# Optimization experiments

Measured on AMD Instinct MI355X. Metric: run time of the kernel, lower is better.

The kernel has to match this reference:

```python
import jax, jax.numpy as jnp
import numpy as np

N = 50000
E = 800000
D_IN, D_HID, D_OUT = 128, 128, 64


def setup_inputs() -> dict:
    key = jax.random.key(0)
    ks = jax.random.split(key, 8)
    x = jax.random.normal(ks[0], (N, D_IN), dtype=jnp.float32)
    edge_index = jax.random.randint(ks[1], (2, E), 0, N, dtype=jnp.int64)
    # Glorot-ish init for GCNConv linear weights + zero bias (PyG default bias=True)
    def lin(k, din, dout):
        s = 1.0 / np.sqrt(din)
        return jax.random.uniform(k, (din, dout), jnp.float32, -s, s)
    return {
        "x": x,
        "edge_index": edge_index,
        "W1": lin(ks[2], D_IN, D_HID), "b1": jnp.zeros((D_HID,), jnp.float32),
        "W2": lin(ks[3], D_HID, D_HID), "b2": jnp.zeros((D_HID,), jnp.float32),
        "W3": lin(ks[4], D_HID, D_OUT), "b3": jnp.zeros((D_OUT,), jnp.float32),
    }


def _prep_edges(edge_index, n):
    # add self loops (PyG GCNConv default add_self_loops=True)
    loop = jnp.arange(n, dtype=edge_index.dtype)
    src = jnp.concatenate([edge_index[0], loop])
    dst = jnp.concatenate([edge_index[1], loop])
    deg = jax.ops.segment_sum(jnp.ones_like(dst, dtype=jnp.float32), dst, num_segments=n)
    dinv = jnp.where(deg > 0, jax.lax.rsqrt(deg), 0.0)
    norm = dinv[src] * dinv[dst]  # symmetric normalization per edge
    return src, dst, norm


def _gcn_conv(h, W, b, src, dst, norm, n):
    h = h @ W                                   # [N, dout]
    msg = h[src] * norm[:, None]                # [E+N, dout] gather
    out = jax.ops.segment_sum(msg, dst, num_segments=n)  # scatter-add
    return out + b


def reference(x, edge_index, W1, b1, W2, b2, W3, b3):
    src, dst, norm = _prep_edges(edge_index, N)
    h = jax.nn.relu(_gcn_conv(x, W1, b1, src, dst, norm, N))
    h = jax.nn.relu(_gcn_conv(h, W2, b2, src, dst, norm, N))
    return _gcn_conv(h, W3, b3, src, dst, norm, N)  # eval mode: dropout is identity
```

## Files before the change

kernel.cpp:

```cpp
#include <hip/hip_runtime.h>
#include <hip/hip_fp16.h>
#include <math.h>

#define NN 50000
#define NE 800000
#define RAWSTRIDE 96
#define NBUCK 196
#define NBBIN 196
#define BCAP 4608
#define ACH 4096
#define G1B 782

using bf8v = __attribute__((ext_vector_type(8))) short;
using f4v  = __attribute__((ext_vector_type(4))) float;

__device__ inline unsigned short f2bf(float f) {
    unsigned int u = __float_as_uint(f);
    u += 0x7FFFu + ((u >> 16) & 1u);
    return (unsigned short)(u >> 16);
}
__device__ inline float bflo(unsigned int d) { return __uint_as_float(d << 16); }
__device__ inline float bfhi(unsigned int d) { return __uint_as_float(d & 0xFFFF0000u); }


__device__ __forceinline__ void bin_body(const int* __restrict__ src,
                                         const int* __restrict__ dst,
                                         int* __restrict__ gcursor,
                                         unsigned int* __restrict__ bst,
                                         int bx, char* shc) {
    unsigned int* items = (unsigned int*)shc;
    int* cnt    = (int*)(shc + 16384);
    int* pref   = (int*)(shc + 17408);
    int* gstart = (int*)(shc + 18436);
    const int t = threadIdx.x;
    cnt[t] = 0;
    __syncthreads();
    const int base = bx * ACH;

    unsigned int my[16]; int myb[16], myr[16];
    #pragma unroll
    for (int i = 0; i < 16; ++i) {
        int e = base + i * 256 + t;
        my[i] = 0; myb[i] = -1; myr[i] = 0;
        if (e < NE) {
            int d = dst[e], s = src[e];
            my[i] = (unsigned int)s | ((unsigned int)d << 16);
            int b = d >> 8;
            myb[i] = b;
            myr[i] = atomicAdd(&cnt[b], 1);
        }
    }
    __syncthreads();
    if (t == 0) {
        int run = 0;
        for (int b = 0; b < 256; ++b) { pref[b] = run; run += cnt[b]; }
        pref[256] = run;
    }
    __syncthreads();
    if (cnt[t] > 0) gstart[t] = atomicAdd(&gcursor[t], cnt[t]);
    __syncthreads();
    #pragma unroll
    for (int i = 0; i < 16; ++i)
        if (myb[i] >= 0) items[pref[myb[i]] + myr[i]] = my[i];
    __syncthreads();
    const int total = pref[256];
    for (int i = t; i < total; i += 256) {
        int lo = 0, hi = 255;
        while (lo < hi) { int mid = (lo + hi + 1) >> 1; if (pref[mid] <= i) lo = mid; else hi = mid - 1; }
        int idx = gstart[lo] + (i - pref[lo]);
        if (idx < BCAP) bst[(size_t)lo * BCAP + idx] = items[i];
    }
}


__global__ __launch_bounds__(512) void sortb_kernel(const int* __restrict__ gcursor,
                                                    const unsigned int* __restrict__ bst,
                                                    int* __restrict__ cnt_g,
                                                    float* __restrict__ dinv,
                                                    unsigned short* __restrict__ raw) {
    __shared__ unsigned int items[BCAP];
    __shared__ int cnt[256], pref[257], cur[256];
    __shared__ unsigned short outl[BCAP];
    const int b = blockIdx.x;
    const int t = threadIdx.x;
    int n = gcursor[b];
    if (n > BCAP) n = BCAP;
    if (t < 256) { cnt[t] = 0; cur[t] = 0; }
    __syncthreads();
    for (int i = t; i < n; i += 512) {
        unsigned int u = bst[(size_t)b * BCAP + i];
        items[i] = u;
        atomicAdd(&cnt[(u >> 16) & 255], 1);
    }
    __syncthreads();
    if (t == 0) {
        int run = 0;
        for (int j = 0; j < 256; ++j) { pref[j] = run; run += cnt[j]; }
        pref[256] = run;
    }
    __syncthreads();
    for (int i = t; i < n; i += 512) {
        unsigned int u = items[i];
        int ln = (u >> 16) & 255;
        int r = atomicAdd(&cur[ln], 1);
        outl[pref[ln] + r] = (unsigned short)(u & 0xFFFFu);
    }
    __syncthreads();
    for (int i = t; i < n; i += 512) {
        int lo = 0, hi = 255;
        while (lo < hi) { int mid = (lo + hi + 1) >> 1; if (pref[mid] <= i) lo = mid; else hi = mid - 1; }
        int r = i - pref[lo];
        if (r < RAWSTRIDE) raw[(size_t)(b * 256 + lo) * RAWSTRIDE + r] = outl[i];
    }
    if (t < 256) {
        int node = b * 256 + t;
        if (node < NN) {
            int c = cnt[t];
            cnt_g[node] = c;
            dinv[node] = rsqrtf((float)(1 + c));
        }
    }
}


template <bool A_FP32>
__device__ __forceinline__ void gemm128_body(const void* __restrict__ Ain,
                                             const float* __restrict__ W,
                                             unsigned short* __restrict__ out,
                                             int bx, char* shc) {
    unsigned short* Wt = (unsigned short*)shc;
    unsigned short* Dt = (unsigned short*)(shc + 128 * 136 * 2);
    const int t = threadIdx.x;
    const int row0 = bx * 64;

    {
        int n = t & 127;
        int kbase = (t >> 7) * 4;
        for (int kk = kbase; kk < 128; kk += 8) {
            float w0 = W[(kk + 0) * 128 + n];
            float w1 = W[(kk + 1) * 128 + n];
            float w2 = W[(kk + 2) * 128 + n];
            float w3 = W[(kk + 3) * 128 + n];
            unsigned int p0 = (unsigned int)f2bf(w0) | ((unsigned int)f2bf(w1) << 16);
            unsigned int p1 = (unsigned int)f2bf(w2) | ((unsigned int)f2bf(w3) << 16);
            *(unsigned int*)&Wt[n * 136 + kk]     = p0;
            *(unsigned int*)&Wt[n * 136 + kk + 2] = p1;
        }
    }
    __syncthreads();

    const int wave = t >> 6;
    const int lane = t & 63;
    const int m16  = lane & 15;
    const int quad = lane >> 4;
    const int arow = row0 + wave * 16 + m16;
    const int arowc = (arow < NN) ? arow : 0;

    f4v acc[8];
    #pragma unroll
    for (int i = 0; i < 8; ++i) acc[i] = (f4v)(0.0f);

    #pragma unroll
    for (int k0 = 0; k0 < 128; k0 += 32) {
        bf8v afrag;
        if (A_FP32) {
            const float* A = (const float*)Ain;
            const float4* ap = (const float4*)(A + (size_t)arowc * 128 + k0 + quad * 8);
            float4 a0 = ap[0], a1 = ap[1];
            afrag[0] = (short)f2bf(a0.x); afrag[1] = (short)f2bf(a0.y);
            afrag[2] = (short)f2bf(a0.z); afrag[3] = (short)f2bf(a0.w);
            afrag[4] = (short)f2bf(a1.x); afrag[5] = (short)f2bf(a1.y);
            afrag[6] = (short)f2bf(a1.z); afrag[7] = (short)f2bf(a1.w);
        } else {
            const unsigned short* A = (const unsigned short*)Ain;
            afrag = *(const bf8v*)(A + (size_t)arowc * 128 + k0 + quad * 8);
        }
        #pragma unroll
        for (int nt = 0; nt < 8; ++nt) {
            bf8v bfrag = *(const bf8v*)&Wt[(nt * 16 + m16) * 136 + k0 + quad * 8];
            acc[nt] = __builtin_amdgcn_mfma_f32_16x16x32_bf16(afrag, bfrag, acc[nt], 0, 0, 0);
        }
    }

    #pragma unroll
    for (int nt = 0; nt < 8; ++nt) {
        #pragma unroll
        for (int r = 0; r < 4; ++r) {
            Dt[(wave * 16 + quad * 4 + r) * 136 + nt * 16 + m16] = f2bf(acc[nt][r]);
        }
    }
    __syncthreads();

    {
        int r = t >> 2;
        int c = t & 3;
        int gr = row0 + r;
        if (gr < NN) {
            const uint4* s = (const uint4*)&Dt[r * 136] + c * 4;
            uint4* d = (uint4*)(out + (size_t)gr * 128) + c * 4;
            d[0] = s[0]; d[1] = s[1]; d[2] = s[2]; d[3] = s[3];
        }
    }
}

__global__ __launch_bounds__(256) void bin_g1_kernel(const int* __restrict__ src,
                                                     const int* __restrict__ dst,
                                                     int* __restrict__ gcursor,
                                                     unsigned int* __restrict__ bst,
                                                     const float* __restrict__ x,
                                                     const float* __restrict__ W1,
                                                     unsigned short* __restrict__ hb) {
    __shared__ __align__(16) char sh[52224];
    if (blockIdx.x < NBBIN) {
        bin_body(src, dst, gcursor, bst, blockIdx.x, sh);
    } else {
        gemm128_body<true>(x, W1, hb, blockIdx.x - NBBIN, sh);
    }
}

__global__ __launch_bounds__(256) void mfma_gemm_kernel(const unsigned short* __restrict__ Ain,
                                                        const float* __restrict__ W,
                                                        unsigned short* __restrict__ out) {
    __shared__ __align__(16) char sh[52224];
    gemm128_body<false>(Ain, W, out, blockIdx.x, sh);
}


template <bool RELU>
__global__ __launch_bounds__(256) void agg_bf16_kernel(const unsigned short* __restrict__ hin,
                                                       const unsigned short* __restrict__ raw,
                                                       const int* __restrict__ cnt_g,
                                                       const float* __restrict__ dinv,
                                                       const float* __restrict__ bias,
                                                       unsigned short* __restrict__ outb) {
    const int t = threadIdx.x;
    const int group = t >> 4;
    const int lane  = t & 15;
    const int wid = blockIdx.x * 16 + group;
    if (wid >= NN) return;

    int c = cnt_g[wid];
    if (c > RAWSTRIDE) c = RAWSTRIDE;
    const float diw = dinv[wid];
    const unsigned short* rrow = raw + (size_t)wid * RAWSTRIDE;
    const uint4* hv = (const uint4*)hin;

    float acc[8];
    {
        uint4 g = hv[(size_t)wid * 16 + lane];
        float ws = diw * diw;
        acc[0] = ws * bflo(g.x); acc[1] = ws * bfhi(g.x);
        acc[2] = ws * bflo(g.y); acc[3] = ws * bfhi(g.y);
        acc[4] = ws * bflo(g.z); acc[5] = ws * bfhi(g.z);
        acc[6] = ws * bflo(g.w); acc[7] = ws * bfhi(g.w);
    }

    #define ACCUM(G, W_) \
        acc[0] += W_ * bflo(G.x); acc[1] += W_ * bfhi(G.x); \
        acc[2] += W_ * bflo(G.y); acc[3] += W_ * bfhi(G.y); \
        acc[4] += W_ * bflo(G.z); acc[5] += W_ * bfhi(G.z); \
        acc[6] += W_ * bflo(G.w); acc[7] += W_ * bfhi(G.w);

    const int cfull = c & ~7;
    uint4 q;
    if (cfull > 0) q = *(const uint4*)(rrow);
    for (int e = 0; e < cfull; e += 8) {
        uint4 qc = q;
        if (e + 8 < cfull) q = *(const uint4*)(rrow + e + 8);
        int c0 = qc.x & 0xFFFFu, c1 = qc.x >> 16;
        int c2 = qc.y & 0xFFFFu, c3 = qc.y >> 16;
        int c4 = qc.z & 0xFFFFu, c5 = qc.z >> 16;
        int c6 = qc.w & 0xFFFFu, c7 = qc.w >> 16;
        uint4 g0 = hv[(size_t)c0 * 16 + lane];
        uint4 g1 = hv[(size_t)c1 * 16 + lane];
        uint4 g2 = hv[(size_t)c2 * 16 + lane];
        uint4 g3 = hv[(size_t)c3 * 16 + lane];
        uint4 g4 = hv[(size_t)c4 * 16 + lane];
        uint4 g5 = hv[(size_t)c5 * 16 + lane];
        uint4 g6 = hv[(size_t)c6 * 16 + lane];
        uint4 g7 = hv[(size_t)c7 * 16 + lane];
        float w0 = diw * dinv[c0], w1 = diw * dinv[c1];
        float w2 = diw * dinv[c2], w3 = diw * dinv[c3];
        float w4 = diw * dinv[c4], w5 = diw * dinv[c5];
        float w6 = diw * dinv[c6], w7 = diw * dinv[c7];
        ACCUM(g0, w0) ACCUM(g1, w1) ACCUM(g2, w2) ACCUM(g3, w3)
        ACCUM(g4, w4) ACCUM(g5, w5) ACCUM(g6, w6) ACCUM(g7, w7)
    }
    if (c & 7) {
        int e = cfull, rem = c - e;
        uint4 qc = *(const uint4*)(rrow + e);
        int c0 = qc.x & 0xFFFFu, c1 = qc.x >> 16;
        int c2 = qc.y & 0xFFFFu, c3 = qc.y >> 16;
        int c4 = qc.z & 0xFFFFu, c5 = qc.z >> 16;
        int c6 = qc.w & 0xFFFFu, c7 = qc.w >> 16;
        if (rem <= 1) c1 = 0; if (rem <= 2) c2 = 0; if (rem <= 3) c3 = 0;
        if (rem <= 4) c4 = 0; if (rem <= 5) c5 = 0; if (rem <= 6) c6 = 0;
        c7 = 0;
        float w0 = diw * dinv[c0];
        float w1 = (rem > 1) ? diw * dinv[c1] : 0.f;
        float w2 = (rem > 2) ? diw * dinv[c2] : 0.f;
        float w3 = (rem > 3) ? diw * dinv[c3] : 0.f;
        float w4 = (rem > 4) ? diw * dinv[c4] : 0.f;
        float w5 = (rem > 5) ? diw * dinv[c5] : 0.f;
        float w6 = (rem > 6) ? diw * dinv[c6] : 0.f;
        float w7 = 0.f;
        uint4 g0 = hv[(size_t)c0 * 16 + lane];
        uint4 g1 = hv[(size_t)c1 * 16 + lane];
        uint4 g2 = hv[(size_t)c2 * 16 + lane];
        uint4 g3 = hv[(size_t)c3 * 16 + lane];
        uint4 g4 = hv[(size_t)c4 * 16 + lane];
        uint4 g5 = hv[(size_t)c5 * 16 + lane];
        uint4 g6 = hv[(size_t)c6 * 16 + lane];
        uint4 g7 = hv[(size_t)c7 * 16 + lane];
        ACCUM(g0, w0) ACCUM(g1, w1) ACCUM(g2, w2) ACCUM(g3, w3)
        ACCUM(g4, w4) ACCUM(g5, w5) ACCUM(g6, w6) ACCUM(g7, w7)
    }
    #undef ACCUM

    const float4* bp = (const float4*)bias;
    float4 b0 = bp[lane * 2], b1 = bp[lane * 2 + 1];
    acc[0] += b0.x; acc[1] += b0.y; acc[2] += b0.z; acc[3] += b0.w;
    acc[4] += b1.x; acc[5] += b1.y; acc[6] += b1.z; acc[7] += b1.w;
    if (RELU) {
        #pragma unroll
        for (int j = 0; j < 8; ++j) acc[j] = fmaxf(acc[j], 0.f);
    }
    uint4 o;
    o.x = (unsigned int)f2bf(acc[0]) | ((unsigned int)f2bf(acc[1]) << 16);
    o.y = (unsigned int)f2bf(acc[2]) | ((unsigned int)f2bf(acc[3]) << 16);
    o.z = (unsigned int)f2bf(acc[4]) | ((unsigned int)f2bf(acc[5]) << 16);
    o.w = (unsigned int)f2bf(acc[6]) | ((unsigned int)f2bf(acc[7]) << 16);
    ((uint4*)(outb + (size_t)wid * 128))[lane] = o;
}


__global__ __launch_bounds__(256) void gemm3_kernel(const unsigned short* __restrict__ Ab,
                                                    const float* __restrict__ W,
                                                    unsigned short* __restrict__ outh) {
    constexpr int CG = 16;
    constexpr int RPT = 4;
    constexpr int ROWS = 64;
    constexpr int LD = 132;
    __shared__ float lds[ROWS * LD];
    const int t = threadIdx.x;
    const int row0 = blockIdx.x * ROWS;

    #pragma unroll
    for (int j = 0; j < ROWS / 8; ++j) {
        int idx4 = j * 256 + t;
        int r = idx4 >> 5, c4 = idx4 & 31;
        int gr = row0 + r;
        uint2 u = make_uint2(0u, 0u);
        if (gr < NN) u = ((const uint2*)(Ab + (size_t)gr * 128))[c4];
        float4 v;
        v.x = bflo(u.x); v.y = bfhi(u.x); v.z = bflo(u.y); v.w = bfhi(u.y);
        ((float4*)(lds + r * LD))[c4] = v;
    }
    __syncthreads();

    const int cg = t % CG;
    const int rt = t / CG;
    const float4* Wv = (const float4*)W;
    float4 acc[RPT];
    #pragma unroll
    for (int i = 0; i < RPT; ++i) acc[i] = make_float4(0.f, 0.f, 0.f, 0.f);

    for (int k0 = 0; k0 < 128; k0 += 4) {
        float4 w0 = Wv[(k0 + 0) * CG + cg];
        float4 w1 = Wv[(k0 + 1) * CG + cg];
        float4 w2 = Wv[(k0 + 2) * CG + cg];
        float4 w3 = Wv[(k0 + 3) * CG + cg];
        #pragma unroll
        for (int i = 0; i < RPT; ++i) {
            const float* lr = lds + (rt * RPT + i) * LD;
            float4 a = ((const float4*)lr)[k0 >> 2];
            acc[i].x += a.x * w0.x + a.y * w1.x + a.z * w2.x + a.w * w3.x;
            acc[i].y += a.x * w0.y + a.y * w1.y + a.z * w2.y + a.w * w3.y;
            acc[i].z += a.x * w0.z + a.y * w1.z + a.z * w2.z + a.w * w3.z;
            acc[i].w += a.x * w0.w + a.y * w1.w + a.z * w2.w + a.w * w3.w;
        }
    }

    #pragma unroll
    for (int i = 0; i < RPT; ++i) {
        int gr = row0 + rt * RPT + i;
        if (gr < NN) {
            uint2 o;
            o.x = (unsigned int)f2bf(acc[i].x) | ((unsigned int)f2bf(acc[i].y) << 16);
            o.y = (unsigned int)f2bf(acc[i].z) | ((unsigned int)f2bf(acc[i].w) << 16);
            ((uint2*)(outh + (size_t)gr * 64))[cg] = o;
        }
    }
}


__global__ __launch_bounds__(256) void agg3_kernel(const unsigned short* __restrict__ hin,
                                                   const unsigned short* __restrict__ raw,
                                                   const int* __restrict__ cnt_g,
                                                   const float* __restrict__ dinv,
                                                   const float* __restrict__ bias,
                                                   float* __restrict__ out) {
    const int t = threadIdx.x;
    const int group = t >> 3;
    const int lane  = t & 7;
    const int wid = blockIdx.x * 32 + group;
    if (wid >= NN) return;

    int c = cnt_g[wid];
    if (c > RAWSTRIDE) c = RAWSTRIDE;
    const float diw = dinv[wid];
    const unsigned short* rrow = raw + (size_t)wid * RAWSTRIDE;
    const uint4* hv = (const uint4*)hin;

    float acc[8];
    {
        uint4 g = hv[(size_t)wid * 8 + lane];
        float ws = diw * diw;
        acc[0] = ws * bflo(g.x); acc[1] = ws * bfhi(g.x);
        acc[2] = ws * bflo(g.y); acc[3] = ws * bfhi(g.y);
        acc[4] = ws * bflo(g.z); acc[5] = ws * bfhi(g.z);
        acc[6] = ws * bflo(g.w); acc[7] = ws * bfhi(g.w);
    }

    #define ACCUM(G, W_) \
        acc[0] += W_ * bflo(G.x); acc[1] += W_ * bfhi(G.x); \
        acc[2] += W_ * bflo(G.y); acc[3] += W_ * bfhi(G.y); \
        acc[4] += W_ * bflo(G.z); acc[5] += W_ * bfhi(G.z); \
        acc[6] += W_ * bflo(G.w); acc[7] += W_ * bfhi(G.w);

    const int cfull = c & ~7;
    uint4 q;
    if (cfull > 0) q = *(const uint4*)(rrow);
    for (int e = 0; e < cfull; e += 8) {
        uint4 qc = q;
        if (e + 8 < cfull) q = *(const uint4*)(rrow + e + 8);
        int c0 = qc.x & 0xFFFFu, c1 = qc.x >> 16;
        int c2 = qc.y & 0xFFFFu, c3 = qc.y >> 16;
        int c4 = qc.z & 0xFFFFu, c5 = qc.z >> 16;
        int c6 = qc.w & 0xFFFFu, c7 = qc.w >> 16;
        uint4 g0 = hv[(size_t)c0 * 8 + lane];
        uint4 g1 = hv[(size_t)c1 * 8 + lane];
        uint4 g2 = hv[(size_t)c2 * 8 + lane];
        uint4 g3 = hv[(size_t)c3 * 8 + lane];
        uint4 g4 = hv[(size_t)c4 * 8 + lane];
        uint4 g5 = hv[(size_t)c5 * 8 + lane];
        uint4 g6 = hv[(size_t)c6 * 8 + lane];
        uint4 g7 = hv[(size_t)c7 * 8 + lane];
        float w0 = diw * dinv[c0], w1 = diw * dinv[c1];
        float w2 = diw * dinv[c2], w3 = diw * dinv[c3];
        float w4 = diw * dinv[c4], w5 = diw * dinv[c5];
        float w6 = diw * dinv[c6], w7 = diw * dinv[c7];
        ACCUM(g0, w0) ACCUM(g1, w1) ACCUM(g2, w2) ACCUM(g3, w3)
        ACCUM(g4, w4) ACCUM(g5, w5) ACCUM(g6, w6) ACCUM(g7, w7)
    }
    if (c & 7) {
        int e = cfull, rem = c - e;
        uint4 qc = *(const uint4*)(rrow + e);
        int c0 = qc.x & 0xFFFFu, c1 = qc.x >> 16;
        int c2 = qc.y & 0xFFFFu, c3 = qc.y >> 16;
        int c4 = qc.z & 0xFFFFu, c5 = qc.z >> 16;
        int c6 = qc.w & 0xFFFFu, c7 = qc.w >> 16;
        if (rem <= 1) c1 = 0; if (rem <= 2) c2 = 0; if (rem <= 3) c3 = 0;
        if (rem <= 4) c4 = 0; if (rem <= 5) c5 = 0; if (rem <= 6) c6 = 0;
        c7 = 0;
        float w0 = diw * dinv[c0];
        float w1 = (rem > 1) ? diw * dinv[c1] : 0.f;
        float w2 = (rem > 2) ? diw * dinv[c2] : 0.f;
        float w3 = (rem > 3) ? diw * dinv[c3] : 0.f;
        float w4 = (rem > 4) ? diw * dinv[c4] : 0.f;
        float w5 = (rem > 5) ? diw * dinv[c5] : 0.f;
        float w6 = (rem > 6) ? diw * dinv[c6] : 0.f;
        float w7 = 0.f;
        uint4 g0 = hv[(size_t)c0 * 8 + lane];
        uint4 g1 = hv[(size_t)c1 * 8 + lane];
        uint4 g2 = hv[(size_t)c2 * 8 + lane];
        uint4 g3 = hv[(size_t)c3 * 8 + lane];
        uint4 g4 = hv[(size_t)c4 * 8 + lane];
        uint4 g5 = hv[(size_t)c5 * 8 + lane];
        uint4 g6 = hv[(size_t)c6 * 8 + lane];
        uint4 g7 = hv[(size_t)c7 * 8 + lane];
        ACCUM(g0, w0) ACCUM(g1, w1) ACCUM(g2, w2) ACCUM(g3, w3)
        ACCUM(g4, w4) ACCUM(g5, w5) ACCUM(g6, w6) ACCUM(g7, w7)
    }
    #undef ACCUM

    const float4* bp = (const float4*)bias;
    float4 b0 = bp[lane * 2], b1 = bp[lane * 2 + 1];
    acc[0] += b0.x; acc[1] += b0.y; acc[2] += b0.z; acc[3] += b0.w;
    acc[4] += b1.x; acc[5] += b1.y; acc[6] += b1.z; acc[7] += b1.w;

    float4 o0 = make_float4(acc[0], acc[1], acc[2], acc[3]);
    float4 o1 = make_float4(acc[4], acc[5], acc[6], acc[7]);
    ((float4*)(out + (size_t)wid * 64))[lane * 2]     = o0;
    ((float4*)(out + (size_t)wid * 64))[lane * 2 + 1] = o1;
}


extern "C" void kernel_launch(void* const* d_in, const int* in_sizes, int n_in,
                              void* d_out, int out_size, void* d_ws, size_t ws_size,
                              hipStream_t stream) {
    const float* x  = (const float*)d_in[0];
    const int*   ei = (const int*)d_in[1];
    const float* W1 = (const float*)d_in[2];
    const float* b1 = (const float*)d_in[3];
    const float* W2 = (const float*)d_in[4];
    const float* b2 = (const float*)d_in[5];
    const float* W3 = (const float*)d_in[6];
    const float* b3 = (const float*)d_in[7];
    float* out = (float*)d_out;

    char* w = (char*)d_ws;
    int*   cnt_g   = (int*)  (w + 0x0000000);
    int*   gcursor = (int*)  (w + 0x0040000);
    float* dinv    = (float*)(w + 0x0048000);
    unsigned int*   bst = (unsigned int*)  (w + 0x0080000);
    unsigned short* raw = (unsigned short*)(w + 0x0400000);
    unsigned short* hb  = (unsigned short*)(w + 0x0E00000);
    unsigned short* zb  = (unsigned short*)(w + 0x1B00000);
    unsigned short* h3b = (unsigned short*)(w + 0x2800000);

    const int* src = ei;
    const int* dst = ei + NE;

    hipMemsetAsync(gcursor, 0, NBUCK * sizeof(int), stream);
    bin_g1_kernel<<<NBBIN + G1B, 256, 0, stream>>>(src, dst, gcursor, bst, x, W1, hb);
    sortb_kernel<<<NBUCK, 512, 0, stream>>>(gcursor, bst, cnt_g, dinv, raw);
    agg_bf16_kernel<true><<<(NN + 15) / 16, 256, 0, stream>>>(hb, raw, cnt_g, dinv, b1, zb);
    mfma_gemm_kernel<<<G1B, 256, 0, stream>>>(zb, W2, hb);
    agg_bf16_kernel<true><<<(NN + 15) / 16, 256, 0, stream>>>(hb, raw, cnt_g, dinv, b2, zb);
    gemm3_kernel<<<G1B, 256, 0, stream>>>(zb, W3, h3b);
    agg3_kernel<<<(NN + 31) / 32, 256, 0, stream>>>(h3b, raw, cnt_g, dinv, b3, out);
}
```

Baseline: 246.7 us.

## Fuse aggregation with following GEMM in layers one and two

Layer-1 aggregation (with bias and ReLU) is merged with the W2 MFMA GEMM into one kernel, and layer-2 aggregation is merged with the W3 GEMM. Aggregated rows now stay in LDS instead of being written to global memory and read back, which also removes two kernel launches. In exchange, each block handles 64 rows serially in four passes of 16, so there are fewer blocks to hide gather latency, the W tile is rebuilt per block, and LDS use per block goes up.

```diff
diff --git a/kernel.cpp b/kernel.cpp
--- a/kernel.cpp
+++ b/kernel.cpp
@@ -123,11 +123,10 @@
 }
 
 
-template <bool A_FP32>
-__device__ __forceinline__ void gemm128_body(const void* __restrict__ Ain,
-                                             const float* __restrict__ W,
-                                             unsigned short* __restrict__ out,
-                                             int bx, char* shc) {
+__device__ __forceinline__ void gemm128_body_f32(const float* __restrict__ A,
+                                                 const float* __restrict__ W,
+                                                 unsigned short* __restrict__ out,
+                                                 int bx, char* shc) {
     unsigned short* Wt = (unsigned short*)shc;
     unsigned short* Dt = (unsigned short*)(shc + 128 * 136 * 2);
     const int t = threadIdx.x;
@@ -163,18 +162,12 @@
     #pragma unroll
     for (int k0 = 0; k0 < 128; k0 += 32) {
         bf8v afrag;
-        if (A_FP32) {
-            const float* A = (const float*)Ain;
-            const float4* ap = (const float4*)(A + (size_t)arowc * 128 + k0 + quad * 8);
-            float4 a0 = ap[0], a1 = ap[1];
-            afrag[0] = (short)f2bf(a0.x); afrag[1] = (short)f2bf(a0.y);
-            afrag[2] = (short)f2bf(a0.z); afrag[3] = (short)f2bf(a0.w);
-            afrag[4] = (short)f2bf(a1.x); afrag[5] = (short)f2bf(a1.y);
-            afrag[6] = (short)f2bf(a1.z); afrag[7] = (short)f2bf(a1.w);
-        } else {
-            const unsigned short* A = (const unsigned short*)Ain;
-            afrag = *(const bf8v*)(A + (size_t)arowc * 128 + k0 + quad * 8);
-        }
+        const float4* ap = (const float4*)(A + (size_t)arowc * 128 + k0 + quad * 8);
+        float4 a0 = ap[0], a1 = ap[1];
+        afrag[0] = (short)f2bf(a0.x); afrag[1] = (short)f2bf(a0.y);
+        afrag[2] = (short)f2bf(a0.z); afrag[3] = (short)f2bf(a0.w);
+        afrag[4] = (short)f2bf(a1.x); afrag[5] = (short)f2bf(a1.y);
+        afrag[6] = (short)f2bf(a1.z); afrag[7] = (short)f2bf(a1.w);
         #pragma unroll
         for (int nt = 0; nt < 8; ++nt) {
             bf8v bfrag = *(const bf8v*)&Wt[(nt * 16 + m16) * 136 + k0 + quad * 8];
@@ -214,150 +207,220 @@
     if (blockIdx.x < NBBIN) {
         bin_body(src, dst, gcursor, bst, blockIdx.x, sh);
     } else {
-        gemm128_body<true>(x, W1, hb, blockIdx.x - NBBIN, sh);
-    }
-}
-
-__global__ __launch_bounds__(256) void mfma_gemm_kernel(const unsigned short* __restrict__ Ain,
-                                                        const float* __restrict__ W,
-                                                        unsigned short* __restrict__ out) {
-    __shared__ __align__(16) char sh[52224];
-    gemm128_body<false>(Ain, W, out, blockIdx.x, sh);
-}
-
-
-template <bool RELU>
-__global__ __launch_bounds__(256) void agg_bf16_kernel(const unsigned short* __restrict__ hin,
-                                                       const unsigned short* __restrict__ raw,
-                                                       const int* __restrict__ cnt_g,
-                                                       const float* __restrict__ dinv,
-                                                       const float* __restrict__ bias,
-                                                       unsigned short* __restrict__ outb) {
+        gemm128_body_f32(x, W1, hb, blockIdx.x - NBBIN, sh);
+    }
+}
+
+
+#define AGG128_BODY(HV, RROW, C, DIW, LANE, ACCV)                                   \
+    {                                                                               \
+        uint4 g = HV[(size_t)wid * 16 + (LANE)];                                    \
+        float ws = (DIW) * (DIW);                                                   \
+        ACCV[0] = ws * bflo(g.x); ACCV[1] = ws * bfhi(g.x);                         \
+        ACCV[2] = ws * bflo(g.y); ACCV[3] = ws * bfhi(g.y);                         \
+        ACCV[4] = ws * bflo(g.z); ACCV[5] = ws * bfhi(g.z);                         \
+        ACCV[6] = ws * bflo(g.w); ACCV[7] = ws * bfhi(g.w);                         \
+    }                                                                               \
+    const int cfull = (C) & ~7;                                                     \
+    uint4 q;                                                                        \
+    if (cfull > 0) q = *(const uint4*)(RROW);                                       \
+    for (int e = 0; e < cfull; e += 8) {                                            \
+        uint4 qc = q;                                                               \
+        if (e + 8 < cfull) q = *(const uint4*)((RROW) + e + 8);                     \
+        int c0 = qc.x & 0xFFFFu, c1 = qc.x >> 16;                                   \
+        int c2 = qc.y & 0xFFFFu, c3 = qc.y >> 16;                                   \
+        int c4 = qc.z & 0xFFFFu, c5 = qc.z >> 16;                                   \
+        int c6 = qc.w & 0xFFFFu, c7 = qc.w >> 16;                                   \
+        uint4 g0 = HV[(size_t)c0 * 16 + (LANE)];                                    \
+        uint4 g1 = HV[(size_t)c1 * 16 + (LANE)];                                    \
+        uint4 g2 = HV[(size_t)c2 * 16 + (LANE)];                                    \
+        uint4 g3 = HV[(size_t)c3 * 16 + (LANE)];                                    \
+        uint4 g4 = HV[(size_t)c4 * 16 + (LANE)];                                    \
+        uint4 g5 = HV[(size_t)c5 * 16 + (LANE)];                                    \
+        uint4 g6 = HV[(size_t)c6 * 16 + (LANE)];                                    \
+        uint4 g7 = HV[(size_t)c7 * 16 + (LANE)];                                    \
+        float w0 = (DIW) * dinv[c0], w1 = (DIW) * dinv[c1];                         \
+        float w2 = (DIW) * dinv[c2], w3 = (DIW) * dinv[c3];                         \
+        float w4 = (DIW) * dinv[c4], w5 = (DIW) * dinv[c5];                         \
+        float w6 = (DIW) * dinv[c6], w7 = (DIW) * dinv[c7];                         \
+        ACC8(g0, w0) ACC8(g1, w1) ACC8(g2, w2) ACC8(g3, w3)                         \
+        ACC8(g4, w4) ACC8(g5, w5) ACC8(g6, w6) ACC8(g7, w7)                         \
+    }                                                                               \
+    if ((C) & 7) {                                                                  \
+        int e = cfull, rem = (C) - e;                                               \
+        uint4 qc = *(const uint4*)((RROW) + e);                                     \
+        int c0 = qc.x & 0xFFFFu, c1 = qc.x >> 16;                                   \
+        int c2 = qc.y & 0xFFFFu, c3 = qc.y >> 16;                                   \
+        int c4 = qc.z & 0xFFFFu, c5 = qc.z >> 16;                                   \
+        int c6 = qc.w & 0xFFFFu, c7 = qc.w >> 16;                                   \
+        if (rem <= 1) c1 = 0; if (rem <= 2) c2 = 0; if (rem <= 3) c3 = 0;           \
+        if (rem <= 4) c4 = 0; if (rem <= 5) c5 = 0; if (rem <= 6) c6 = 0;           \
+        c7 = 0;                                                                     \
+        float w0 = (DIW) * dinv[c0];                                                \
+        float w1 = (rem > 1) ? (DIW) * dinv[c1] : 0.f;                              \
+        float w2 = (rem > 2) ? (DIW) * dinv[c2] : 0.f;                              \
+        float w3 = (rem > 3) ? (DIW) * dinv[c3] : 0.f;                              \
+        float w4 = (rem > 4) ? (DIW) * dinv[c4] : 0.f;                              \
+        float w5 = (rem > 5) ? (DIW) * dinv[c5] : 0.f;                              \
+        float w6 = (rem > 6) ? (DIW) * dinv[c6] : 0.f;                              \
+        float w7 = 0.f;                                                             \
+        uint4 g0 = HV[(size_t)c0 * 16 + (LANE)];                                    \
+        uint4 g1 = HV[(size_t)c1 * 16 + (LANE)];                                    \
+        uint4 g2 = HV[(size_t)c2 * 16 + (LANE)];                                    \
+        uint4 g3 = HV[(size_t)c3 * 16 + (LANE)];                                    \
+        uint4 g4 = HV[(size_t)c4 * 16 + (LANE)];                                    \
+        uint4 g5 = HV[(size_t)c5 * 16 + (LANE)];                                    \
+        uint4 g6 = HV[(size_t)c6 * 16 + (LANE)];                                    \
+        uint4 g7 = HV[(size_t)c7 * 16 + (LANE)];                                    \
+        ACC8(g0, w0) ACC8(g1, w1) ACC8(g2, w2) ACC8(g3, w3)                         \
+        ACC8(g4, w4) ACC8(g5, w5) ACC8(g6, w6) ACC8(g7, w7)                         \
+    }
+
+#define ACC8(G, W_) \
+    acc[0] += W_ * bflo(G.x); acc[1] += W_ * bfhi(G.x); \
+    acc[2] += W_ * bflo(G.y); acc[3] += W_ * bfhi(G.y); \
+    acc[4] += W_ * bflo(G.z); acc[5] += W_ * bfhi(G.z); \
+    acc[6] += W_ * bflo(G.w); acc[7] += W_ * bfhi(G.w);
+
+
+__global__ __launch_bounds__(256) void aggW2_kernel(const unsigned short* __restrict__ hin,
+                                                    const unsigned short* __restrict__ raw,
+                                                    const int* __restrict__ cnt_g,
+                                                    const float* __restrict__ dinv,
+                                                    const float* __restrict__ bias,
+                                                    const float* __restrict__ W,
+                                                    unsigned short* __restrict__ out) {
+    __shared__ unsigned short Wt[128 * 136];
+    __shared__ unsigned short Zt[64 * 136];
     const int t = threadIdx.x;
+    const int row0 = blockIdx.x * 64;
+
+    {
+        int n = t & 127;
+        int kbase = (t >> 7) * 4;
+        for (int kk = kbase; kk < 128; kk += 8) {
+            float w0 = W[(kk + 0) * 128 + n];
+            float w1 = W[(kk + 1) * 128 + n];
+            float w2 = W[(kk + 2) * 128 + n];
+            float w3 = W[(kk + 3) * 128 + n];
+            unsigned int p0 = (unsigned int)f2bf(w0) | ((unsigned int)f2bf(w1) << 16);
+            unsigned int p1 = (unsigned int)f2bf(w2) | ((unsigned int)f2bf(w3) << 16);
+            *(unsigned int*)&Wt[n * 136 + kk]     = p0;
+            *(unsigned int*)&Wt[n * 136 + kk + 2] = p1;
+        }
+    }
+
     const int group = t >> 4;
     const int lane  = t & 15;
-    const int wid = blockIdx.x * 16 + group;
-    if (wid >= NN) return;
-
-    int c = cnt_g[wid];
-    if (c > RAWSTRIDE) c = RAWSTRIDE;
-    const float diw = dinv[wid];
-    const unsigned short* rrow = raw + (size_t)wid * RAWSTRIDE;
     const uint4* hv = (const uint4*)hin;
-
-    float acc[8];
-    {
-        uint4 g = hv[(size_t)wid * 16 + lane];
-        float ws = diw * diw;
-        acc[0] = ws * bflo(g.x); acc[1] = ws * bfhi(g.x);
-        acc[2] = ws * bflo(g.y); acc[3] = ws * bfhi(g.y);
-        acc[4] = ws * bflo(g.z); acc[5] = ws * bfhi(g.z);
-        acc[6] = ws * bflo(g.w); acc[7] = ws * bfhi(g.w);
-    }
-
-    #define ACCUM(G, W_) \
-        acc[0] += W_ * bflo(G.x); acc[1] += W_ * bfhi(G.x); \
-        acc[2] += W_ * bflo(G.y); acc[3] += W_ * bfhi(G.y); \
-        acc[4] += W_ * bflo(G.z); acc[5] += W_ * bfhi(G.z); \
-        acc[6] += W_ * bflo(G.w); acc[7] += W_ * bfhi(G.w);
-
-    const int cfull = c & ~7;
-    uint4 q;
-    if (cfull > 0) q = *(const uint4*)(rrow);
-    for (int e = 0; e < cfull; e += 8) {
-        uint4 qc = q;
-        if (e + 8 < cfull) q = *(const uint4*)(rrow + e + 8);
-        int c0 = qc.x & 0xFFFFu, c1 = qc.x >> 16;
-        int c2 = qc.y & 0xFFFFu, c3 = qc.y >> 16;
-        int c4 = qc.z & 0xFFFFu, c5 = qc.z >> 16;
-        int c6 = qc.w & 0xFFFFu, c7 = qc.w >> 16;
-        uint4 g0 = hv[(size_t)c0 * 16 + lane];
-        uint4 g1 = hv[(size_t)c1 * 16 + lane];
-        uint4 g2 = hv[(size_t)c2 * 16 + lane];
-        uint4 g3 = hv[(size_t)c3 * 16 + lane];
-        uint4 g4 = hv[(size_t)c4 * 16 + lane];
-        uint4 g5 = hv[(size_t)c5 * 16 + lane];
-        uint4 g6 = hv[(size_t)c6 * 16 + lane];
-        uint4 g7 = hv[(size_t)c7 * 16 + lane];
-        float w0 = diw * dinv[c0], w1 = diw * dinv[c1];
-        float w2 = diw * dinv[c2], w3 = diw * dinv[c3];
-        float w4 = diw * dinv[c4], w5 = diw * dinv[c5];
-        float w6 = diw * dinv[c6], w7 = diw * dinv[c7];
-        ACCUM(g0, w0) ACCUM(g1, w1) ACCUM(g2, w2) ACCUM(g3, w3)
-        ACCUM(g4, w4) ACCUM(g5, w5) ACCUM(g6, w6) ACCUM(g7, w7)
-    }
-    if (c & 7) {
-        int e = cfull, rem = c - e;
-        uint4 qc = *(const uint4*)(rrow + e);
-        int c0 = qc.x & 0xFFFFu, c1 = qc.x >> 16;
-        int c2 = qc.y & 0xFFFFu, c3 = qc.y >> 16;
-        int c4 = qc.z & 0xFFFFu, c5 = qc.z >> 16;
-        int c6 = qc.w & 0xFFFFu, c7 = qc.w >> 16;
-        if (rem <= 1) c1 = 0; if (rem <= 2) c2 = 0; if (rem <= 3) c3 = 0;
-        if (rem <= 4) c4 = 0; if (rem <= 5) c5 = 0; if (rem <= 6) c6 = 0;
-        c7 = 0;
-        float w0 = diw * dinv[c0];
-        float w1 = (rem > 1) ? diw * dinv[c1] : 0.f;
-        float w2 = (rem > 2) ? diw * dinv[c2] : 0.f;
-        float w3 = (rem > 3) ? diw * dinv[c3] : 0.f;
-        float w4 = (rem > 4) ? diw * dinv[c4] : 0.f;
-        float w5 = (rem > 5) ? diw * dinv[c5] : 0.f;
-        float w6 = (rem > 6) ? diw * dinv[c6] : 0.f;
-        float w7 = 0.f;
-        uint4 g0 = hv[(size_t)c0 * 16 + lane];
-        uint4 g1 = hv[(size_t)c1 * 16 + lane];
-        uint4 g2 = hv[(size_t)c2 * 16 + lane];
-        uint4 g3 = hv[(size_t)c3 * 16 + lane];
-        uint4 g4 = hv[(size_t)c4 * 16 + lane];
-        uint4 g5 = hv[(size_t)c5 * 16 + lane];
-        uint4 g6 = hv[(size_t)c6 * 16 + lane];
-        uint4 g7 = hv[(size_t)c7 * 16 + lane];
-        ACCUM(g0, w0) ACCUM(g1, w1) ACCUM(g2, w2) ACCUM(g3, w3)
-        ACCUM(g4, w4) ACCUM(g5, w5) ACCUM(g6, w6) ACCUM(g7, w7)
-    }
-    #undef ACCUM
-
     const float4* bp = (const float4*)bias;
     float4 b0 = bp[lane * 2], b1 = bp[lane * 2 + 1];
-    acc[0] += b0.x; acc[1] += b0.y; acc[2] += b0.z; acc[3] += b0.w;
-    acc[4] += b1.x; acc[5] += b1.y; acc[6] += b1.z; acc[7] += b1.w;
-    if (RELU) {
+
+    for (int r = 0; r < 4; ++r) {
+        const int wid = row0 + r * 16 + group;
+        uint4 o = make_uint4(0u, 0u, 0u, 0u);
+        if (wid < NN) {
+            int c = cnt_g[wid];
+            if (c > RAWSTRIDE) c = RAWSTRIDE;
+            const float diw = dinv[wid];
+            const unsigned short* rrow = raw + (size_t)wid * RAWSTRIDE;
+            float acc[8];
+            AGG128_BODY(hv, rrow, c, diw, lane, acc)
+            acc[0] += b0.x; acc[1] += b0.y; acc[2] += b0.z; acc[3] += b0.w;
+            acc[4] += b1.x; acc[5] += b1.y; acc[6] += b1.z; acc[7] += b1.w;
+            #pragma unroll
+            for (int j = 0; j < 8; ++j) acc[j] = fmaxf(acc[j], 0.f);
+            o.x = (unsigned int)f2bf(acc[0]) | ((unsigned int)f2bf(acc[1]) << 16);
+            o.y = (unsigned int)f2bf(acc[2]) | ((unsigned int)f2bf(acc[3]) << 16);
+            o.z = (unsigned int)f2bf(acc[4]) | ((unsigned int)f2bf(acc[5]) << 16);
+            o.w = (unsigned int)f2bf(acc[6]) | ((unsigned int)f2bf(acc[7]) << 16);
+        }
+        *(uint4*)&Zt[(r * 16 + group) * 136 + lane * 8] = o;
+    }
+    __syncthreads();
+
+    const int wave = t >> 6;
+    const int l64  = t & 63;
+    const int m16  = l64 & 15;
+    const int quad = l64 >> 4;
+
+    f4v acc[8];
+    #pragma unroll
+    for (int i = 0; i < 8; ++i) acc[i] = (f4v)(0.0f);
+
+    #pragma unroll
+    for (int k0 = 0; k0 < 128; k0 += 32) {
+        bf8v afrag = *(const bf8v*)&Zt[(wave * 16 + m16) * 136 + k0 + quad * 8];
         #pragma unroll
-        for (int j = 0; j < 8; ++j) acc[j] = fmaxf(acc[j], 0.f);
-    }
-    uint4 o;
-    o.x = (unsigned int)f2bf(acc[0]) | ((unsigned int)f2bf(acc[1]) << 16);
-    o.y = (unsigned int)f2bf(acc[2]) | ((unsigned int)f2bf(acc[3]) << 16);
-    o.z = (unsigned int)f2bf(acc[4]) | ((unsigned int)f2bf(acc[5]) << 16);
-    o.w = (unsigned int)f2bf(acc[6]) | ((unsigned int)f2bf(acc[7]) << 16);
-    ((uint4*)(outb + (size_t)wid * 128))[lane] = o;
-}
-
-
-__global__ __launch_bounds__(256) void gemm3_kernel(const unsigned short* __restrict__ Ab,
+        for (int nt = 0; nt < 8; ++nt) {
+            bf8v bfrag = *(const bf8v*)&Wt[(nt * 16 + m16) * 136 + k0 + quad * 8];
+            acc[nt] = __builtin_amdgcn_mfma_f32_16x16x32_bf16(afrag, bfrag, acc[nt], 0, 0, 0);
+        }
+    }
+    __syncthreads();
+
+    #pragma unroll
+    for (int nt = 0; nt < 8; ++nt) {
+        #pragma unroll
+        for (int r = 0; r < 4; ++r) {
+            Zt[(wave * 16 + quad * 4 + r) * 136 + nt * 16 + m16] = f2bf(acc[nt][r]);
+        }
+    }
+    __syncthreads();
+
+    {
+        int r = t >> 2;
+        int c = t & 3;
+        int gr = row0 + r;
+        if (gr < NN) {
+            const uint4* s = (const uint4*)&Zt[r * 136] + c * 4;
+            uint4* d = (uint4*)(out + (size_t)gr * 128) + c * 4;
+            d[0] = s[0]; d[1] = s[1]; d[2] = s[2]; d[3] = s[3];
+        }
+    }
+}
+
+
+__global__ __launch_bounds__(256) void aggG3_kernel(const unsigned short* __restrict__ hin,
+                                                    const unsigned short* __restrict__ raw,
+                                                    const int* __restrict__ cnt_g,
+                                                    const float* __restrict__ dinv,
+                                                    const float* __restrict__ bias,
                                                     const float* __restrict__ W,
                                                     unsigned short* __restrict__ outh) {
+    constexpr int LD = 132;
+    __shared__ float Zt[64 * LD];
+    const int t = threadIdx.x;
+    const int row0 = blockIdx.x * 64;
+
+    const int group = t >> 4;
+    const int lane  = t & 15;
+    const uint4* hv = (const uint4*)hin;
+    const float4* bp = (const float4*)bias;
+    float4 b0 = bp[lane * 2], b1 = bp[lane * 2 + 1];
+
+    for (int r = 0; r < 4; ++r) {
+        const int wid = row0 + r * 16 + group;
+        float acc[8] = {0.f, 0.f, 0.f, 0.f, 0.f, 0.f, 0.f, 0.f};
+        if (wid < NN) {
+            int c = cnt_g[wid];
+            if (c > RAWSTRIDE) c = RAWSTRIDE;
+            const float diw = dinv[wid];
+            const unsigned short* rrow = raw + (size_t)wid * RAWSTRIDE;
+            AGG128_BODY(hv, rrow, c, diw, lane, acc)
+            acc[0] += b0.x; acc[1] += b0.y; acc[2] += b0.z; acc[3] += b0.w;
+            acc[4] += b1.x; acc[5] += b1.y; acc[6] += b1.z; acc[7] += b1.w;
+            #pragma unroll
+            for (int j = 0; j < 8; ++j) acc[j] = fmaxf(acc[j], 0.f);
+        }
+        float4* zr = (float4*)&Zt[(r * 16 + group) * LD + lane * 8];
+        zr[0] = make_float4(acc[0], acc[1], acc[2], acc[3]);
+        zr[1] = make_float4(acc[4], acc[5], acc[6], acc[7]);
+    }
+    __syncthreads();
+
     constexpr int CG = 16;
     constexpr int RPT = 4;
-    constexpr int ROWS = 64;
-    constexpr int LD = 132;
-    __shared__ float lds[ROWS * LD];
-    const int t = threadIdx.x;
-    const int row0 = blockIdx.x * ROWS;
-
-    #pragma unroll
-    for (int j = 0; j < ROWS / 8; ++j) {
-        int idx4 = j * 256 + t;
-        int r = idx4 >> 5, c4 = idx4 & 31;
-        int gr = row0 + r;
-        uint2 u = make_uint2(0u, 0u);
-        if (gr < NN) u = ((const uint2*)(Ab + (size_t)gr * 128))[c4];
-        float4 v;
-        v.x = bflo(u.x); v.y = bfhi(u.x); v.z = bflo(u.y); v.w = bfhi(u.y);
-        ((float4*)(lds + r * LD))[c4] = v;
-    }
-    __syncthreads();
-
     const int cg = t % CG;
     const int rt = t / CG;
     const float4* Wv = (const float4*)W;
@@ -372,7 +435,7 @@
         float4 w3 = Wv[(k0 + 3) * CG + cg];
         #pragma unroll
         for (int i = 0; i < RPT; ++i) {
-            const float* lr = lds + (rt * RPT + i) * LD;
+            const float* lr = Zt + (rt * RPT + i) * LD;
             float4 a = ((const float4*)lr)[k0 >> 2];
             acc[i].x += a.x * w0.x + a.y * w1.x + a.z * w2.x + a.w * w3.x;
             acc[i].y += a.x * w0.y + a.y * w1.y + a.z * w2.y + a.w * w3.y;
@@ -421,12 +484,6 @@
         acc[4] = ws * bflo(g.z); acc[5] = ws * bfhi(g.z);
         acc[6] = ws * bflo(g.w); acc[7] = ws * bfhi(g.w);
     }
-
-    #define ACCUM(G, W_) \
-        acc[0] += W_ * bflo(G.x); acc[1] += W_ * bfhi(G.x); \
-        acc[2] += W_ * bflo(G.y); acc[3] += W_ * bfhi(G.y); \
-        acc[4] += W_ * bflo(G.z); acc[5] += W_ * bfhi(G.z); \
-        acc[6] += W_ * bflo(G.w); acc[7] += W_ * bfhi(G.w);
 
     const int cfull = c & ~7;
     uint4 q;
@@ -450,8 +507,8 @@
         float w2 = diw * dinv[c2], w3 = diw * dinv[c3];
         float w4 = diw * dinv[c4], w5 = diw * dinv[c5];
         float w6 = diw * dinv[c6], w7 = diw * dinv[c7];
-        ACCUM(g0, w0) ACCUM(g1, w1) ACCUM(g2, w2) ACCUM(g3, w3)
-        ACCUM(g4, w4) ACCUM(g5, w5) ACCUM(g6, w6) ACCUM(g7, w7)
+        ACC8(g0, w0) ACC8(g1, w1) ACC8(g2, w2) ACC8(g3, w3)
+        ACC8(g4, w4) ACC8(g5, w5) ACC8(g6, w6) ACC8(g7, w7)
     }
     if (c & 7) {
         int e = cfull, rem = c - e;
@@ -479,10 +536,9 @@
         uint4 g5 = hv[(size_t)c5 * 8 + lane];
         uint4 g6 = hv[(size_t)c6 * 8 + lane];
         uint4 g7 = hv[(size_t)c7 * 8 + lane];
-        ACCUM(g0, w0) ACCUM(g1, w1) ACCUM(g2, w2) ACCUM(g3, w3)
-        ACCUM(g4, w4) ACCUM(g5, w5) ACCUM(g6, w6) ACCUM(g7, w7)
-    }
-    #undef ACCUM
+        ACC8(g0, w0) ACC8(g1, w1) ACC8(g2, w2) ACC8(g3, w3)
+        ACC8(g4, w4) ACC8(g5, w5) ACC8(g6, w6) ACC8(g7, w7)
+    }
 
     const float4* bp = (const float4*)bias;
     float4 b0 = bp[lane * 2], b1 = bp[lane * 2 + 1];
@@ -516,7 +572,7 @@
     unsigned int*   bst = (unsigned int*)  (w + 0x0080000);
     unsigned short* raw = (unsigned short*)(w + 0x0400000);
     unsigned short* hb  = (unsigned short*)(w + 0x0E00000);
-    unsigned short* zb  = (unsigned short*)(w + 0x1B00000);
+    unsigned short* h2b = (unsigned short*)(w + 0x1B00000);
     unsigned short* h3b = (unsigned short*)(w + 0x2800000);
 
     const int* src = ei;
@@ -525,9 +581,7 @@
     hipMemsetAsync(gcursor, 0, NBUCK * sizeof(int), stream);
     bin_g1_kernel<<<NBBIN + G1B, 256, 0, stream>>>(src, dst, gcursor, bst, x, W1, hb);
     sortb_kernel<<<NBUCK, 512, 0, stream>>>(gcursor, bst, cnt_g, dinv, raw);
-    agg_bf16_kernel<true><<<(NN + 15) / 16, 256, 0, stream>>>(hb, raw, cnt_g, dinv, b1, zb);
-    mfma_gemm_kernel<<<G1B, 256, 0, stream>>>(zb, W2, hb);
-    agg_bf16_kernel<true><<<(NN + 15) / 16, 256, 0, stream>>>(hb, raw, cnt_g, dinv, b2, zb);
-    gemm3_kernel<<<G1B, 256, 0, stream>>>(zb, W3, h3b);
+    aggW2_kernel<<<G1B, 256, 0, stream>>>(hb, raw, cnt_g, dinv, b1, W2, h2b);
+    aggG3_kernel<<<G1B, 256, 0, stream>>>(h2b, raw, cnt_g, dinv, b2, W3, h3b);
     agg3_kernel<<<(NN + 31) / 32, 256, 0, stream>>>(h3b, raw, cnt_g, dinv, b3, out);
 }
```

New measurement: 239.4 us. 2.9% less time.
